# Kernel optimization log

Hardware: AMD Instinct MI355X
Metric: run time of the kernel (lower is better)

Reference implementation:

```python
import jax, jax.numpy as jnp
import numpy as np

# B batch, N seq (n_vec), V vocab, D model dim, H heads, DH head dim,
# L depth, WS window size, R landmark rank, C classes
B, N, V, D, H, DH, L, WS, R, C = 4, 4096, 512, 512, 8, 64, 4, 128, 256, 10
FF = 4 * D
SCALE = DH ** -0.5


def _ln(t, g, b, eps=1e-5):
    mu = jnp.mean(t, axis=-1, keepdims=True)
    var = jnp.var(t, axis=-1, keepdims=True)
    return (t - mu) * jax.lax.rsqrt(var + eps) * g + b


def setup_inputs():
    key = jax.random.key(0)
    ks = iter(jax.random.split(key, 16))

    def w(shape, s=0.02):
        return (jax.random.normal(next(ks), shape) * s).astype(jnp.float32)

    return dict(
        x=jax.random.randint(next(ks), (B, N), 0, V, dtype=jnp.int32),
        tok_emb=w((V, D)), pos_emb=w((N, D)),
        ln1_g=jnp.ones((L, D), jnp.float32), ln1_b=jnp.zeros((L, D), jnp.float32),
        Wq=w((L, D, H * DH)), Wkv=w((L, D, 2 * H * DH)), Wp=w((L, DH, R)),
        lln_g=jnp.ones((L, DH), jnp.float32), lln_b=jnp.zeros((L, DH), jnp.float32),
        gln_g=jnp.ones((L, DH), jnp.float32), gln_b=jnp.zeros((L, DH), jnp.float32),
        Wo=w((L, H * DH, D)), bo=jnp.zeros((L, D), jnp.float32),
        ln2_g=jnp.ones((L, D), jnp.float32), ln2_b=jnp.zeros((L, D), jnp.float32),
        W1=w((L, D, FF)), b1=jnp.zeros((L, FF), jnp.float32),
        W2=w((L, FF, D)), b2=jnp.zeros((L, D), jnp.float32),
        lnf_g=jnp.ones((D,), jnp.float32), lnf_b=jnp.zeros((D,), jnp.float32),
        Wlog=w((D, V)), blog=jnp.zeros((V,), jnp.float32),
        Wfin=w((N * V, C), 0.005), bfin=jnp.zeros((C,), jnp.float32),
    )


def _forward(x, tok_emb, pos_emb, ln1_g, ln1_b, Wq, Wkv, Wp, lln_g, lln_b,
             gln_g, gln_b, Wo, bo, ln2_g, ln2_b, W1, b1, W2, b2,
             lnf_g, lnf_b, Wlog, blog, Wfin, bfin):
    h = tok_emb[x] + pos_emb[None, :, :]  # [B,N,D]
    nw = N // WS
    for l in range(L):
        # ---- PreNorm Long-Short attention ----
        y = _ln(h, ln1_g[l], ln1_b[l])
        q = (y @ Wq[l]).reshape(B, N, H, DH).transpose(0, 2, 1, 3) * SCALE  # [B,H,N,DH]
        kv = (y @ Wkv[l]).reshape(B, N, 2, H, DH).transpose(2, 0, 3, 1, 4)
        k, v = kv[0], kv[1]  # [B,H,N,DH]
        # dynamic low-rank landmark projection: softmax over the sequence dim
        p = jax.nn.softmax(jnp.einsum('bhnd,dr->bhnr', k, Wp[l]), axis=2)
        gk = _ln(jnp.einsum('bhnr,bhnd->bhrd', p, k), gln_g[l], gln_b[l])  # [B,H,R,DH]
        gv = _ln(jnp.einsum('bhnr,bhnd->bhrd', p, v), gln_g[l], gln_b[l])
        # DualLN on the short-range (local window) keys/values
        lk = _ln(k, lln_g[l], lln_b[l]).reshape(B, H, nw, WS, DH)
        lv = _ln(v, lln_g[l], lln_b[l]).reshape(B, H, nw, WS, DH)
        lq = q.reshape(B, H, nw, WS, DH)
        sim_l = jnp.einsum('bhnwd,bhnxd->bhnwx', lq, lk)  # [B,H,nw,WS,WS]
        sim_g = jnp.einsum('bhnwd,bhrd->bhnwr', lq, gk)   # [B,H,nw,WS,R]
        attn = jax.nn.softmax(jnp.concatenate([sim_l, sim_g], axis=-1), axis=-1)
        a_l, a_g = attn[..., :WS], attn[..., WS:]
        o = (jnp.einsum('bhnwx,bhnxd->bhnwd', a_l, lv)
             + jnp.einsum('bhnwr,bhrd->bhnwd', a_g, gv))
        o = o.reshape(B, H, N, DH).transpose(0, 2, 1, 3).reshape(B, N, H * DH)
        h = h + o @ Wo[l] + bo[l]
        # ---- PreNorm FeedForward ----
        y = _ln(h, ln2_g[l], ln2_b[l])
        h = h + jax.nn.gelu(y @ W1[l] + b1[l]) @ W2[l] + b2[l]
    logits = _ln(h, lnf_g, lnf_b) @ Wlog + blog  # [B,N,V]
    # FLATTEN pooling head (dropout is identity in eval mode)
    return logits.reshape(B, N * V) @ Wfin + bfin  # [B,C]


def reference(x, tok_emb, pos_emb, ln1_g, ln1_b, Wq, Wkv, Wp, lln_g, lln_b,
              gln_g, gln_b, Wo, bo, ln2_g, ln2_b, W1, b1, W2, b2,
              lnf_g, lnf_b, Wlog, blog, Wfin, bfin):
    return _forward(x, tok_emb, pos_emb, ln1_g, ln1_b, Wq, Wkv, Wp, lln_g, lln_b,
                    gln_g, gln_b, Wo, bo, ln2_g, ln2_b, W1, b1, W2, b2,
                    lnf_g, lnf_b, Wlog, blog, Wfin, bfin)
```

## Files before the change

### kernel.cpp

```cpp
#include <hip/hip_runtime.h>
#include <hip/hip_bf16.h>

typedef unsigned short u16;
typedef __attribute__((ext_vector_type(8))) short short8;
typedef __attribute__((ext_vector_type(4))) float floatx4;

#define FLAG_GELU   1
#define FLAG_ACC    2
#define FLAG_NN     4
#define FLAG_CF32   8
#define FLAG_ATOMIC 16

__device__ __forceinline__ float bf2f(u16 u){
  union { unsigned u; float f; } c; c.u = ((unsigned)u)<<16; return c.f;
}
__device__ __forceinline__ u16 f2bf(float f){
  union { float f; unsigned u; } c; c.f = f;
  unsigned r = (c.u + 0x7fffu + ((c.u>>16)&1u))>>16;
  return (u16)r;
}
__device__ __forceinline__ float rdin(const void* base, long long idx, int flagv){
  return flagv ? ((const float*)base)[idx] : bf2f(((const u16*)base)[idx]);
}
__device__ __forceinline__ float fast_gelu(float x){
  float u = 0.7978845608028654f*(x + 0.044715f*x*x*x);
  float e = __expf(2.f*u);
  float t = 1.f - 2.f/(e+1.f);
  return 0.5f*x*(1.f+t);
}

__global__ void detect_kernel(const void* tok, int* flag){
  __shared__ int cnt;
  if(threadIdx.x==0) cnt=0;
  __syncthreads();
  float v = fabsf(bf2f(((const u16*)tok)[threadIdx.x]));
  int bad = (v < 1e3f) ? 0 : 1;
  atomicAdd(&cnt, bad);
  __syncthreads();
  if(threadIdx.x==0) *flag = (cnt>0) ? 1 : 0;
}

__global__ void cvtT_kernel(const void* src, long long off0, long long zstride, u16* __restrict__ dst,
    long long dzstride, int K, int N, const int* flag){
  __shared__ float tl[32][33];
  int fl = *flag;
  int k0 = blockIdx.x*32, n0 = blockIdx.y*32;
  long long base = off0 + (long long)blockIdx.z*zstride;
  for(int i=threadIdx.y;i<32;i+=8){
    long long idx = base + (long long)(k0+i)*N + n0 + threadIdx.x;
    tl[i][threadIdx.x] = fl ? ((const float*)src)[idx] : bf2f(((const u16*)src)[idx]);
  }
  __syncthreads();
  u16* dz = dst + (long long)blockIdx.z*dzstride;
  for(int i=threadIdx.y;i<32;i+=8)
    dz[(long long)(n0+i)*K + k0 + threadIdx.x] = f2bf(tl[threadIdx.x][i]);
}

__global__ void transposeB_kernel(const u16* __restrict__ in, u16* __restrict__ out,
    long long izs0, long long izs1, int zd, long long ozstride, int ldin, int ldout){
  __shared__ u16 tl[32][33];
  int z = blockIdx.z; int z0 = z/zd, z1 = z - z0*zd;
  const u16* ip = in + z0*izs0 + z1*izs1;
  u16* op = out + (long long)z*ozstride;
  int r0 = blockIdx.x*32, c0 = blockIdx.y*32;
  for(int i=threadIdx.y;i<32;i+=8)
    tl[i][threadIdx.x] = ip[(long long)(r0+i)*ldin + c0 + threadIdx.x];
  __syncthreads();
  for(int i=threadIdx.y;i<32;i+=8)
    op[(long long)(c0+i)*ldout + r0 + threadIdx.x] = tl[threadIdx.x][i];
}

__global__ __launch_bounds__(256) void zerof_kernel(float* p, int n){
  int i = blockIdx.x*256 + threadIdx.x;
  if(i<n) p[i]=0.f;
}

struct GemmP {
  const u16* A; const u16* B; float* Cf; u16* Ch;
  const void* bias; int biasOff; const int* dflag;
  int K, lda, ldb, ldc;
  long long sA0,sA1,sA2,sB0,sB1,sB2,sC0,sC1,sC2;
  int d0,d1; float alpha; int flags; int ksplit;
};

__global__ __launch_bounds__(256) void gemm_kernel(GemmP p){
  __shared__ __align__(16) u16 As[64][40];
  __shared__ __align__(16) u16 Bs[64][40];
  int z = blockIdx.z;
  int i0 = z / p.d0; int rem = z - i0*p.d0; int i1 = rem / p.d1; int i2 = rem - i1*p.d1;
  const u16* A  = p.A + i0*p.sA0 + i1*p.sA1 + i2*p.sA2;
  const u16* Bp = p.B + i0*p.sB0 + i1*p.sB1 + i2*p.sB2;
  long long cb = i0*p.sC0 + i1*p.sC1 + i2*p.sC2;
  int kbeg = 0, kend = p.K;
  if(p.ksplit){ kbeg = i1*p.ksplit; kend = kbeg + p.ksplit; }
  int m0 = blockIdx.x*64, n0 = blockIdx.y*64;
  int t = threadIdx.x, lane = t&63, wave = t>>6;
  int wm = (wave>>1)*32, wn = (wave&1)*32;
  int quad = lane>>4, l16 = lane&15;
  floatx4 zero4 = {0.f,0.f,0.f,0.f};
  floatx4 acc00=zero4, acc01=zero4, acc10=zero4, acc11=zero4;
  int sr = t>>2, sc = (t&3)*8;
  int bkr = t>>3, bnc = (t&7)*8;
  bool nn = (p.flags & FLAG_NN);
  for(int k0=kbeg;k0<kend;k0+=32){
    uint4 av = *(const uint4*)(A + (long long)(m0+sr)*p.lda + (k0+sc));
    uint4 bv;
    if(nn) bv = *(const uint4*)(Bp + (long long)(k0+bkr)*p.ldb + (n0+bnc));
    else   bv = *(const uint4*)(Bp + (long long)(n0+sr)*p.ldb + (k0+sc));
    *(uint4*)&As[sr][sc] = av;
    if(nn){
      u16 tmp[8]; *(uint4*)tmp = bv;
      #pragma unroll
      for(int j=0;j<8;j++) Bs[bnc+j][bkr] = tmp[j];
    } else {
      *(uint4*)&Bs[sr][sc] = bv;
    }
    __syncthreads();
    short8 a0 = *(const short8*)&As[wm+l16][quad*8];
    short8 a1 = *(const short8*)&As[wm+16+l16][quad*8];
    short8 b0 = *(const short8*)&Bs[wn+l16][quad*8];
    short8 b1 = *(const short8*)&Bs[wn+16+l16][quad*8];
    acc00 = __builtin_amdgcn_mfma_f32_16x16x32_bf16(a0,b0,acc00,0,0,0);
    acc01 = __builtin_amdgcn_mfma_f32_16x16x32_bf16(a0,b1,acc01,0,0,0);
    acc10 = __builtin_amdgcn_mfma_f32_16x16x32_bf16(a1,b0,acc10,0,0,0);
    acc11 = __builtin_amdgcn_mfma_f32_16x16x32_bf16(a1,b1,acc11,0,0,0);
    __syncthreads();
  }
  int flagv = p.bias ? *p.dflag : 0;
  #pragma unroll
  for(int mi=0;mi<2;mi++){
    #pragma unroll
    for(int ni=0;ni<2;ni++){
      floatx4 a = (mi==0)?((ni==0)?acc00:acc01):((ni==0)?acc10:acc11);
      int cg = n0 + wn + ni*16 + l16;
      float bv_ = p.bias ? rdin(p.bias, (long long)p.biasOff + cg, flagv) : 0.f;
      #pragma unroll
      for(int e=0;e<4;e++){
        int rg = m0 + wm + mi*16 + quad*4 + e;
        float v = a[e]*p.alpha + bv_;
        if(p.flags & FLAG_GELU) v = fast_gelu(v);
        long long ci = cb + (long long)rg*p.ldc + cg;
        if(p.flags & FLAG_ATOMIC){
          atomicAdd(&p.Cf[ci], v);
        } else if(p.flags & FLAG_CF32){
          float o2 = v; if(p.flags&FLAG_ACC) o2 += p.Cf[ci];
          p.Cf[ci] = o2;
        } else {
          float o2 = v; if(p.flags&FLAG_ACC) o2 += bf2f(p.Ch[ci]);
          p.Ch[ci] = f2bf(o2);
        }
      }
    }
  }
}

struct Gemm128P {
  const u16* A; const u16* B; float* Cf; u16* Ch;
  const void* bias; int biasOff; const int* dflag;
  int K, lda, ldb, ldc; float alpha; int flags;
};

__global__ __launch_bounds__(256) void gemm128_kernel(Gemm128P p){
  __shared__ __align__(16) u16 lds[17408];
  u16* As = lds;
  u16* Bs = lds + 4096;
  int m0 = blockIdx.x*128, n0 = blockIdx.y*128;
  int t = threadIdx.x, lane = t&63, wave = t>>6;
  int quad = lane>>4, l16 = lane&15;
  int wm = (wave>>1)*64, wn = (wave&1)*64;
  int srow = wave*32 + (lane>>2);
  int skoff = (lane&3)*8;
  const u16* Ag0 = p.A + (long long)(m0+srow)*p.lda + skoff;
  const u16* Ag1 = Ag0 + 16*p.lda;
  const u16* Bg0 = p.B + (long long)(n0+srow)*p.ldb + skoff;
  const u16* Bg1 = Bg0 + 16*p.ldb;
  u16* AsW0 = As + wave*1024;
  u16* AsW1 = AsW0 + 512;
  u16* BsW0 = Bs + wave*1024;
  u16* BsW1 = BsW0 + 512;
  floatx4 acc[4][4] = {};
  for(int k0=0;k0<p.K;k0+=32){
    __builtin_amdgcn_global_load_lds(
      (const __attribute__((address_space(1))) unsigned int*)(Ag0 + k0),
      (__attribute__((address_space(3))) unsigned int*)AsW0, 16, 0, 0);
    __builtin_amdgcn_global_load_lds(
      (const __attribute__((address_space(1))) unsigned int*)(Ag1 + k0),
      (__attribute__((address_space(3))) unsigned int*)AsW1, 16, 0, 0);
    __builtin_amdgcn_global_load_lds(
      (const __attribute__((address_space(1))) unsigned int*)(Bg0 + k0),
      (__attribute__((address_space(3))) unsigned int*)BsW0, 16, 0, 0);
    __builtin_amdgcn_global_load_lds(
      (const __attribute__((address_space(1))) unsigned int*)(Bg1 + k0),
      (__attribute__((address_space(3))) unsigned int*)BsW1, 16, 0, 0);
    __syncthreads();
    short8 af[4], bfr[4];
    #pragma unroll
    for(int i=0;i<4;i++) af[i]  = *(const short8*)&As[(wm+i*16+l16)*32 + quad*8];
    #pragma unroll
    for(int j=0;j<4;j++) bfr[j] = *(const short8*)&Bs[(wn+j*16+l16)*32 + quad*8];
    #pragma unroll
    for(int i=0;i<4;i++)
      #pragma unroll
      for(int j=0;j<4;j++)
        acc[i][j] = __builtin_amdgcn_mfma_f32_16x16x32_bf16(af[i], bfr[j], acc[i][j],0,0,0);
    __syncthreads();
  }
  int flagv = p.bias ? *p.dflag : 0;
  if(!(p.flags & FLAG_CF32)){
    u16* Ct = lds + wave*4352;
    #pragma unroll
    for(int j=0;j<4;j++){
      int cg = n0 + wn + j*16 + l16;
      float bv_ = p.bias ? rdin(p.bias, (long long)p.biasOff + cg, flagv) : 0.f;
      #pragma unroll
      for(int i=0;i<4;i++){
        #pragma unroll
        for(int e=0;e<4;e++){
          float v = acc[i][j][e]*p.alpha + bv_;
          if(p.flags & FLAG_GELU) v = fast_gelu(v);
          Ct[(i*16 + quad*4 + e)*68 + j*16 + l16] = f2bf(v);
        }
      }
    }
    int rsub = lane>>3, csub = (lane&7)*8;
    #pragma unroll
    for(int rr=0; rr<8; rr++){
      int row = rr*8 + rsub;
      uint4 v = *(const uint4*)&Ct[row*68 + csub];
      *(uint4*)(p.Ch + (long long)(m0+wm+row)*p.ldc + (n0+wn+csub)) = v;
    }
  } else {
    #pragma unroll
    for(int j=0;j<4;j++){
      int cg = n0 + wn + j*16 + l16;
      float bv_ = p.bias ? rdin(p.bias, (long long)p.biasOff + cg, flagv) : 0.f;
      #pragma unroll
      for(int i=0;i<4;i++){
        #pragma unroll
        for(int e=0;e<4;e++){
          int rg = m0 + wm + i*16 + quad*4 + e;
          float v = acc[i][j][e]*p.alpha + bv_;
          if(p.flags & FLAG_GELU) v = fast_gelu(v);
          long long ci = (long long)rg*p.ldc + cg;
          float o2 = v; if(p.flags&FLAG_ACC) o2 += p.Cf[ci];
          p.Cf[ci] = o2;
        }
      }
    }
  }
}

struct AttnP {
  const u16* q;
  const u16* k;
  const u16* gk;
  const u16* vT;
  const u16* gvT;
  u16* o;
};

__global__ __launch_bounds__(256) void attn_kernel(AttnP p){
  __shared__ __align__(16) u16 S[4][12544];
  __shared__ float ssum[4][32];
  const int SST = 392;
  int w = blockIdx.x, bh = blockIdx.y;
  int b = bh>>3, hh = bh&7;
  int t = threadIdx.x, lane = t&63, wave = t>>6;
  int quad = lane>>4, l16 = lane&15;
  u16* Sw = &S[wave][0];
  int mbase = w*128 + wave*32;
  short8 aq[2][2];
  #pragma unroll
  for(int mt=0;mt<2;mt++)
    #pragma unroll
    for(int kc=0;kc<2;kc++)
      aq[mt][kc] = *(const short8*)(p.q + ((long long)b*4096 + mbase + mt*16 + l16)*512 + hh*64 + kc*32 + quad*8);
  for(int ct=0; ct<24; ct++){
    short8 bf0, bf1;
    if(ct<8){
      const u16* kr = p.k + ((long long)b*4096 + w*128 + ct*16 + l16)*1024 + hh*64;
      bf0 = *(const short8*)(kr + quad*8);
      bf1 = *(const short8*)(kr + 32 + quad*8);
    } else {
      const u16* gr = p.gk + ((long long)bh*256 + (ct-8)*16 + l16)*64;
      bf0 = *(const short8*)(gr + quad*8);
      bf1 = *(const short8*)(gr + 32 + quad*8);
    }
    #pragma unroll
    for(int mt=0;mt<2;mt++){
      floatx4 acc = {0.f,0.f,0.f,0.f};
      acc = __builtin_amdgcn_mfma_f32_16x16x32_bf16(aq[mt][0], bf0, acc,0,0,0);
      acc = __builtin_amdgcn_mfma_f32_16x16x32_bf16(aq[mt][1], bf1, acc,0,0,0);
      #pragma unroll
      for(int e=0;e<4;e++)
        Sw[(mt*16 + quad*4 + e)*SST + ct*16 + l16] = f2bf(acc[e]);
    }
  }
  __syncthreads();
  {
    int r = lane&31, ph = lane>>5;
    u16* Srow = Sw + r*SST + ph*192;
    float mmax = -3.4e38f;
    u16 buf[8];
    for(int it=0; it<24; it++){
      *(uint4*)buf = *(const uint4*)(Srow + it*8);
      #pragma unroll
      for(int j=0;j<8;j++) mmax = fmaxf(mmax, bf2f(buf[j]));
    }
    mmax = fmaxf(mmax, __shfl_xor(mmax, 32));
    float s = 0.f;
    for(int it=0; it<24; it++){
      *(uint4*)buf = *(const uint4*)(Srow + it*8);
      #pragma unroll
      for(int j=0;j<8;j++){ float e_ = __expf(bf2f(buf[j]) - mmax); s += e_; buf[j] = f2bf(e_); }
      *(uint4*)(Srow + it*8) = *(uint4*)buf;
    }
    s += __shfl_xor(s, 32);
    if(ph==0) ssum[wave][r] = 1.f/s;
  }
  __syncthreads();
  floatx4 oacc[2][4] = {};
  for(int kc=0; kc<12; kc++){
    short8 ap0 = *(const short8*)(Sw + (l16)*SST + kc*32 + quad*8);
    short8 ap1 = *(const short8*)(Sw + (16 + l16)*SST + kc*32 + quad*8);
    #pragma unroll
    for(int dt=0; dt<4; dt++){
      short8 bv;
      if(kc<4)
        bv = *(const short8*)(p.vT + (long long)bh*262144 + (dt*16+l16)*4096 + w*128 + kc*32 + quad*8);
      else
        bv = *(const short8*)(p.gvT + (long long)bh*16384 + (dt*16+l16)*256 + (kc-4)*32 + quad*8);
      oacc[0][dt] = __builtin_amdgcn_mfma_f32_16x16x32_bf16(ap0, bv, oacc[0][dt],0,0,0);
      oacc[1][dt] = __builtin_amdgcn_mfma_f32_16x16x32_bf16(ap1, bv, oacc[1][dt],0,0,0);
    }
  }
  #pragma unroll
  for(int mt=0;mt<2;mt++){
    #pragma unroll
    for(int e=0;e<4;e++){
      int row = mt*16 + quad*4 + e;
      float inv = ssum[wave][row];
      long long obase = ((long long)b*4096 + mbase + row)*512 + hh*64;
      #pragma unroll
      for(int dt=0;dt<4;dt++)
        p.o[obase + dt*16 + l16] = f2bf(oacc[mt][dt][e]*inv);
    }
  }
}

__global__ __launch_bounds__(256) void embed_kernel(const int* __restrict__ x, const void* tok,
    const void* pos, float* __restrict__ h, const int* flag){
  int i = blockIdx.x*256 + threadIdx.x;
  int flagv = *flag;
  int d = i & 511;
  int n = (i>>9) & 4095;
  int bn = i>>9;
  int tid2 = x[bn];
  h[i] = rdin(tok, (long long)tid2*512 + d, flagv) + rdin(pos, (long long)n*512 + d, flagv);
}

__global__ __launch_bounds__(256) void ln512_kernel(const float* __restrict__ h,
    const void* g, const void* b, int goff, u16* __restrict__ y, const int* flag){
  int row = blockIdx.x;
  int flagv = *flag;
  const float* hr = h + (size_t)row*512;
  int t = threadIdx.x;
  float x0 = hr[t], x1 = hr[t+256];
  float s1 = x0+x1, s2 = x0*x0+x1*x1;
  for(int o=32;o>0;o>>=1){ s1 += __shfl_down(s1,o,64); s2 += __shfl_down(s2,o,64); }
  __shared__ float sh1[4], sh2[4];
  int wv=t>>6, ln=t&63;
  if(ln==0){ sh1[wv]=s1; sh2[wv]=s2; }
  __syncthreads();
  float st = sh1[0]+sh1[1]+sh1[2]+sh1[3];
  float qt = sh2[0]+sh2[1]+sh2[2]+sh2[3];
  float mu = st*(1.f/512.f);
  float var = qt*(1.f/512.f) - mu*mu;
  float inv = rsqrtf(var+1e-5f);
  u16* yr = y + (size_t)row*512;
  yr[t]     = f2bf((x0-mu)*inv*rdin(g,goff+t,flagv)     + rdin(b,goff+t,flagv));
  yr[t+256] = f2bf((x1-mu)*inv*rdin(g,goff+t+256,flagv) + rdin(b,goff+t+256,flagv));
}

__global__ __launch_bounds__(256) void ln64_kernel(const u16* __restrict__ in, const float* __restrict__ inF,
    u16* __restrict__ out, const void* g, const void* b, int goff,
    long long s0, long long s1v, long long s2v, int d0, int d1, const int* flag){
  int r = blockIdx.x*4 + (threadIdx.x>>6);
  int ln = threadIdx.x&63;
  int flagv = *flag;
  int i0 = r/d0; int rem = r - i0*d0; int i1 = rem/d1; int i2 = rem - i1*d1;
  long long off = i0*s0 + i1*s1v + i2*s2v;
  float x = inF ? inF[off+ln] : bf2f(in[off + ln]);
  float s = x, sq = x*x;
  for(int o=32;o>0;o>>=1){ s += __shfl_down(s,o,64); sq += __shfl_down(sq,o,64); }
  s = __shfl(s,0,64); sq = __shfl(sq,0,64);
  float mu = s*(1.f/64.f), var = sq*(1.f/64.f)-mu*mu;
  float inv = rsqrtf(var+1e-5f);
  out[off + ln] = f2bf((x-mu)*inv*rdin(g,goff+ln,flagv) + rdin(b,goff+ln,flagv));
}

__global__ __launch_bounds__(256) void softmax4096_kernel(u16* __restrict__ p){
  u16* pr = p + (size_t)blockIdx.x*4096;
  int t = threadIdx.x;
  u16 tmp[16];
  *(uint4*)tmp     = *(const uint4*)(pr + t*16);
  *(uint4*)(tmp+8) = *(const uint4*)(pr + t*16 + 8);
  float xs[16]; float m=-3.4e38f;
  #pragma unroll
  for(int i=0;i<16;i++){ xs[i]=bf2f(tmp[i]); m=fmaxf(m,xs[i]); }
  for(int o=32;o>0;o>>=1) m = fmaxf(m, __shfl_down(m,o,64));
  __shared__ float sm[4]; __shared__ float sv[4];
  int wv=t>>6, ln=t&63;
  if(ln==0) sm[wv]=m;
  __syncthreads();
  m = fmaxf(fmaxf(sm[0],sm[1]),fmaxf(sm[2],sm[3]));
  float s=0;
  #pragma unroll
  for(int i=0;i<16;i++){ xs[i]=__expf(xs[i]-m); s+=xs[i]; }
  for(int o=32;o>0;o>>=1) s += __shfl_down(s,o,64);
  if(ln==0) sv[wv]=s;
  __syncthreads();
  s = sv[0]+sv[1]+sv[2]+sv[3];
  float inv = 1.f/s;
  #pragma unroll
  for(int i=0;i<16;i++) tmp[i]=f2bf(xs[i]*inv);
  *(uint4*)(pr + t*16)     = *(uint4*)tmp;
  *(uint4*)(pr + t*16 + 8) = *(uint4*)(tmp+8);
}

__global__ void zero40_kernel(float* p){ if(threadIdx.x<40) p[threadIdx.x]=0.f; }

__global__ __launch_bounds__(256) void head_kernel(const float* __restrict__ logits,
    const void* wfin, float* __restrict__ part, const int* flag){
  int b = blockIdx.x>>7, chunk = blockIdx.x&127;
  int flagv = *flag;
  const float* lr = logits + (size_t)b*2097152 + (size_t)chunk*16384;
  float acc[10];
  #pragma unroll
  for(int c=0;c<10;c++) acc[c]=0.f;
  for(int j=threadIdx.x;j<16384;j+=256){
    float lv_ = lr[j];
    long long wb = (long long)(chunk*16384 + j)*10;
    if(flagv){
      const float* w = (const float*)wfin + wb;
      #pragma unroll
      for(int c=0;c<10;c++) acc[c] += lv_*w[c];
    } else {
      const u16* w = (const u16*)wfin + wb;
      #pragma unroll
      for(int c=0;c<10;c++) acc[c] += lv_*bf2f(w[c]);
    }
  }
  __shared__ float red[4];
  int wv=threadIdx.x>>6, ln=threadIdx.x&63;
  for(int c=0;c<10;c++){
    float v=acc[c];
    for(int o=32;o>0;o>>=1) v+=__shfl_down(v,o,64);
    __syncthreads();
    if(ln==0) red[wv]=v;
    __syncthreads();
    if(threadIdx.x==0) atomicAdd(&part[b*10+c], red[0]+red[1]+red[2]+red[3]);
  }
}

__global__ void fin_kernel(const float* __restrict__ part, const void* bfin, void* out, const int* flag){
  int i=threadIdx.x;
  int flagv = *flag;
  if(i<40){
    float r = part[i] + rdin(bfin, i%10, flagv);
    if(flagv) ((float*)out)[i] = r;
    else      ((u16*)out)[i]   = f2bf(r);
  }
}

static const size_t OFF_H    = 0;
static const size_t OFF_Y    = 33554432;
static const size_t OFF_GKF  = 33554432;
static const size_t OFF_GVF  = 35651584;
static const size_t OFF_Q    = 50331648;
static const size_t OFF_KV   = 67108864;
static const size_t OFF_GK   = 100663296;
static const size_t OFF_GV   = 101711872;
static const size_t OFF_BIG  = 102760448;
static const size_t OFF_KT   = 169869312;
static const size_t OFF_VT   = 186646528;
static const size_t OFF_WTP  = 203423744;
static const size_t OFF_WQT  = 203554816;
static const size_t OFF_WKVT = 204079104;
static const size_t OFF_WOT  = 205127680;
static const size_t OFF_W1T  = 205651968;
static const size_t OFF_W2T  = 207749120;
static const size_t OFF_PART = 209846272;
static const size_t OFF_FLAG = 209846528;
static const size_t WS_NEED  = 209846784;

static inline GemmP mkg(const void*A,const void*B,void*C,const void*bias,int biasOff,const int* dflag,
  int K,int lda,int ldb,int ldc,
  long long a0,long long a1,long long a2,long long b0,long long b1,long long b2,
  long long c0,long long c1,long long c2,int d0,int d1,float alpha,int flags,int ksplit){
  GemmP p; p.A=(const u16*)A; p.B=(const u16*)B;
  p.Cf=(float*)C; p.Ch=(u16*)C; p.bias=bias; p.biasOff=biasOff; p.dflag=dflag;
  p.K=K;p.lda=lda;p.ldb=ldb;p.ldc=ldc;
  p.sA0=a0;p.sA1=a1;p.sA2=a2;p.sB0=b0;p.sB1=b1;p.sB2=b2;p.sC0=c0;p.sC1=c1;p.sC2=c2;
  p.d0=d0;p.d1=d1;p.alpha=alpha;p.flags=flags;p.ksplit=ksplit; return p;
}
static inline Gemm128P mk128(const void*A,const void*B,void*C,const void*bias,int biasOff,const int* dflag,
  int K,int lda,int ldb,int ldc,float alpha,int flags){
  Gemm128P p; p.A=(const u16*)A; p.B=(const u16*)B;
  p.Cf=(float*)C; p.Ch=(u16*)C; p.bias=bias; p.biasOff=biasOff; p.dflag=dflag;
  p.K=K;p.lda=lda;p.ldb=ldb;p.ldc=ldc;p.alpha=alpha;p.flags=flags; return p;
}

extern "C" void kernel_launch(void* const* d_in, const int* in_sizes, int n_in,
                              void* d_out, int out_size, void* d_ws, size_t ws_size,
                              hipStream_t stream){
  (void)in_sizes;(void)n_in;(void)out_size;
  if(ws_size < WS_NEED) return;
  const int*  x    = (const int*)d_in[0];
  const void* tok  = d_in[1];
  const void* pos  = d_in[2];
  const void* ln1g = d_in[3];
  const void* ln1b = d_in[4];
  const void* Wq   = d_in[5];
  const void* Wkv  = d_in[6];
  const void* Wp   = d_in[7];
  const void* llng = d_in[8];
  const void* llnb = d_in[9];
  const void* glng = d_in[10];
  const void* glnb = d_in[11];
  const void* Wo   = d_in[12];
  const void* bo   = d_in[13];
  const void* ln2g = d_in[14];
  const void* ln2b = d_in[15];
  const void* W1   = d_in[16];
  const void* b1   = d_in[17];
  const void* W2   = d_in[18];
  const void* b2   = d_in[19];
  const void* lnfg = d_in[20];
  const void* lnfb = d_in[21];
  const void* Wlog = d_in[22];
  const void* blog = d_in[23];
  const void* Wfin = d_in[24];
  const void* bfin = d_in[25];

  char* ws = (char*)d_ws;
  float* h    = (float*)(ws + OFF_H);
  u16* y      = (u16*)(ws + OFF_Y);
  u16* ob     = (u16*)(ws + OFF_Y);
  float* gkF  = (float*)(ws + OFF_GKF);
  float* gvF  = (float*)(ws + OFF_GVF);
  u16* qb     = (u16*)(ws + OFF_Q);
  u16* kv     = (u16*)(ws + OFF_KV);
  u16* gk     = (u16*)(ws + OFF_GK);
  u16* gv     = (u16*)(ws + OFF_GV);
  u16* big    = (u16*)(ws + OFF_BIG);
  float* bigf = (float*)(ws + OFF_BIG);
  u16* kT     = (u16*)(ws + OFF_KT);
  u16* gvT    = (u16*)(ws + OFF_KT);
  u16* vT     = (u16*)(ws + OFF_VT);
  u16* wTp    = (u16*)(ws + OFF_WTP);
  u16* sWqT   = (u16*)(ws + OFF_WQT);
  u16* sWkvT  = (u16*)(ws + OFF_WKVT);
  u16* sWoT   = (u16*)(ws + OFF_WOT);
  u16* sW1T   = (u16*)(ws + OFF_W1T);
  u16* sW2T   = (u16*)(ws + OFF_W2T);
  float* part = (float*)(ws + OFF_PART);
  int* flag   = (int*)(ws + OFF_FLAG);

  dim3 tb(32,8);
  detect_kernel<<<dim3(1),dim3(256),0,stream>>>(tok, flag);
  cvtT_kernel<<<dim3(2,8,4),tb,0,stream>>>(Wp, 0, 16384, wTp, 16384, 64, 256, flag);
  embed_kernel<<<dim3(32768),dim3(256),0,stream>>>(x, tok, pos, h, flag);

  for(int l=0;l<4;l++){
    cvtT_kernel<<<dim3(16,16,1),tb,0,stream>>>(Wq,  (long long)l*262144,  0, sWqT,  0, 512, 512,  flag);
    cvtT_kernel<<<dim3(16,32,1),tb,0,stream>>>(Wkv, (long long)l*524288,  0, sWkvT, 0, 512, 1024, flag);
    cvtT_kernel<<<dim3(16,16,1),tb,0,stream>>>(Wo,  (long long)l*262144,  0, sWoT,  0, 512, 512,  flag);
    cvtT_kernel<<<dim3(16,64,1),tb,0,stream>>>(W1,  (long long)l*1048576, 0, sW1T,  0, 512, 2048, flag);
    cvtT_kernel<<<dim3(64,16,1),tb,0,stream>>>(W2,  (long long)l*1048576, 0, sW2T,  0, 2048, 512, flag);

    ln512_kernel<<<dim3(16384),dim3(256),0,stream>>>(h, ln1g, ln1b, l*512, y, flag);
    { Gemm128P p = mk128(y, sWqT, qb, nullptr,0,flag, 512,512,512,512, 0.125f, 0);
      gemm128_kernel<<<dim3(128,4),256,0,stream>>>(p); }
    { Gemm128P p = mk128(y, sWkvT, kv, nullptr,0,flag, 512,512,512,1024, 1.f, 0);
      gemm128_kernel<<<dim3(128,8),256,0,stream>>>(p); }
    zerof_kernel<<<dim3(4096),dim3(256),0,stream>>>(gkF, 1048576);
    { GemmP p = mkg(wTp + (size_t)l*16384, kv, big, nullptr,0,flag, 64,64,1024,4096,
        0,0,0, 4194304LL,64,0, 8388608LL,1048576LL,0, 8,1, 1.f, 0, 0);
      gemm_kernel<<<dim3(4,64,32),256,0,stream>>>(p); }
    softmax4096_kernel<<<dim3(8192),dim3(256),0,stream>>>(big);
    transposeB_kernel<<<dim3(128,2,32),tb,0,stream>>>(kv,     kT, 4194304LL,64,8, 262144LL, 1024, 4096);
    transposeB_kernel<<<dim3(128,2,32),tb,0,stream>>>(kv+512, vT, 4194304LL,64,8, 262144LL, 1024, 4096);
    { GemmP p = mkg(big, kT, gkF, nullptr,0,flag, 4096,4096,4096,64,
        1048576LL,0,0, 262144LL,0,0, 16384LL,0,0, 8,1, 1.f, FLAG_CF32|FLAG_ATOMIC, 512);
      gemm_kernel<<<dim3(4,1,256),256,0,stream>>>(p); }
    { GemmP p = mkg(big, vT, gvF, nullptr,0,flag, 4096,4096,4096,64,
        1048576LL,0,0, 262144LL,0,0, 16384LL,0,0, 8,1, 1.f, FLAG_CF32|FLAG_ATOMIC, 512);
      gemm_kernel<<<dim3(4,1,256),256,0,stream>>>(p); }
    ln64_kernel<<<dim3(2048),dim3(256),0,stream>>>(gk, gkF, gk, glng, glnb, l*64, 64,1,1, 1,1, flag);
    ln64_kernel<<<dim3(2048),dim3(256),0,stream>>>(gv, gvF, gv, glng, glnb, l*64, 64,1,1, 1,1, flag);
    ln64_kernel<<<dim3(32768),dim3(256),0,stream>>>(kv,     nullptr, kv,     llng, llnb, l*64, 4194304LL,64,1024, 32768,4096, flag);
    ln64_kernel<<<dim3(32768),dim3(256),0,stream>>>(kv+512, nullptr, kv+512, llng, llnb, l*64, 4194304LL,64,1024, 32768,4096, flag);
    transposeB_kernel<<<dim3(128,2,32),tb,0,stream>>>(kv+512, vT, 4194304LL,64,8, 262144LL, 1024, 4096);
    transposeB_kernel<<<dim3(8,2,32),tb,0,stream>>>(gv, gvT, 16384LL,0,1, 16384LL, 64, 256);
    { AttnP ap; ap.q=qb; ap.k=kv; ap.gk=gk; ap.vT=vT; ap.gvT=gvT; ap.o=ob;
      attn_kernel<<<dim3(32,32),256,0,stream>>>(ap); }
    { Gemm128P p = mk128(ob, sWoT, h, bo,l*512,flag, 512,512,512,512, 1.f, FLAG_ACC|FLAG_CF32);
      gemm128_kernel<<<dim3(128,4),256,0,stream>>>(p); }
    ln512_kernel<<<dim3(16384),dim3(256),0,stream>>>(h, ln2g, ln2b, l*512, y, flag);
    { Gemm128P p = mk128(y, sW1T, big, b1,l*2048,flag, 512,512,512,2048, 1.f, FLAG_GELU);
      gemm128_kernel<<<dim3(128,16),256,0,stream>>>(p); }
    { Gemm128P p = mk128(big, sW2T, h, b2,l*512,flag, 2048,2048,2048,512, 1.f, FLAG_ACC|FLAG_CF32);
      gemm128_kernel<<<dim3(128,4),256,0,stream>>>(p); }
  }
  ln512_kernel<<<dim3(16384),dim3(256),0,stream>>>(h, lnfg, lnfb, 0, y, flag);
  cvtT_kernel<<<dim3(16,16,1),tb,0,stream>>>(Wlog, 0, 0, sWqT, 0, 512, 512, flag);
  { Gemm128P p = mk128(y, sWqT, bigf, blog,0,flag, 512,512,512,512, 1.f, FLAG_CF32);
    gemm128_kernel<<<dim3(128,4),256,0,stream>>>(p); }
  zero40_kernel<<<dim3(1),dim3(64),0,stream>>>(part);
  head_kernel<<<dim3(512),dim3(256),0,stream>>>(bigf, Wfin, part, flag);
  fin_kernel<<<dim3(1),dim3(64),0,stream>>>(part, bfin, d_out, flag);
}
```

Measured before the change: 2.644 ms.

## Replace dense GEMMs with double-buffered 512-thread kernel using larger tiles

Replaces the single-buffered 128x128 GEMM with a templated kernel that uses 8 waves, a 256-wide N tile and BM of 128 or 256, plus a K step of 64. It double-buffers the LDS tiles, so the next K slice loads asynchronously while MFMAs run on the current one, and it needs one barrier per iteration instead of two. Larger tiles improve operand reuse and cut global traffic per FLOP. In exchange, the grids are smaller, leaving fewer blocks to fill the CUs, and LDS use is higher (up to about 136KB for BM=256), which limits occupancy.

```diff
diff --git a/kernel.cpp b/kernel.cpp
--- a/kernel.cpp
+++ b/kernel.cpp
@@ -160,60 +160,79 @@
   int K, lda, ldb, ldc; float alpha; int flags;
 };
 
-__global__ __launch_bounds__(256) void gemm128_kernel(Gemm128P p){
-  __shared__ __align__(16) u16 lds[17408];
+template<int BM>
+__global__ __launch_bounds__(512) void gemm2ph_kernel(Gemm128P p){
+  constexpr int NA   = BM/64;
+  constexpr int HH   = BM/2;
+  constexpr int MI   = HH/16;
+  constexpr int ABUF = BM*64;
+  constexpr int LDSZ = (BM==256) ? 69632 : 49152;
+  __shared__ __align__(16) u16 lds[LDSZ];
   u16* As = lds;
-  u16* Bs = lds + 4096;
-  int m0 = blockIdx.x*128, n0 = blockIdx.y*128;
+  u16* Bs = lds + 2*ABUF;
+  int m0 = blockIdx.x*BM, n0 = blockIdx.y*256;
   int t = threadIdx.x, lane = t&63, wave = t>>6;
   int quad = lane>>4, l16 = lane&15;
-  int wm = (wave>>1)*64, wn = (wave&1)*64;
-  int srow = wave*32 + (lane>>2);
-  int skoff = (lane&3)*8;
-  const u16* Ag0 = p.A + (long long)(m0+srow)*p.lda + skoff;
-  const u16* Ag1 = Ag0 + 16*p.lda;
-  const u16* Bg0 = p.B + (long long)(n0+srow)*p.ldb + skoff;
-  const u16* Bg1 = Bg0 + 16*p.ldb;
-  u16* AsW0 = As + wave*1024;
-  u16* AsW1 = AsW0 + 512;
-  u16* BsW0 = Bs + wave*1024;
-  u16* BsW1 = BsW0 + 512;
-  floatx4 acc[4][4] = {};
-  for(int k0=0;k0<p.K;k0+=32){
-    __builtin_amdgcn_global_load_lds(
-      (const __attribute__((address_space(1))) unsigned int*)(Ag0 + k0),
-      (__attribute__((address_space(3))) unsigned int*)AsW0, 16, 0, 0);
-    __builtin_amdgcn_global_load_lds(
-      (const __attribute__((address_space(1))) unsigned int*)(Ag1 + k0),
-      (__attribute__((address_space(3))) unsigned int*)AsW1, 16, 0, 0);
-    __builtin_amdgcn_global_load_lds(
-      (const __attribute__((address_space(1))) unsigned int*)(Bg0 + k0),
-      (__attribute__((address_space(3))) unsigned int*)BsW0, 16, 0, 0);
-    __builtin_amdgcn_global_load_lds(
-      (const __attribute__((address_space(1))) unsigned int*)(Bg1 + k0),
-      (__attribute__((address_space(3))) unsigned int*)BsW1, 16, 0, 0);
+  int wr = wave>>2, wc = wave&3;
+  int rowA = t>>3, colk = (t&7)*8;
+  const u16* Asrc[NA];
+  const u16* Bsrc[4];
+  #pragma unroll
+  for(int q=0;q<NA;q++) Asrc[q] = p.A + (long long)(m0 + q*64 + rowA)*p.lda + colk;
+  #pragma unroll
+  for(int q=0;q<4;q++)  Bsrc[q] = p.B + (long long)(n0 + q*64 + rowA)*p.ldb + colk;
+  int nk = p.K >> 6;
+  floatx4 acc[MI][4] = {};
+
+  auto stage = [&](int buf, int k0){
+    #pragma unroll
+    for(int q=0;q<NA;q++)
+      __builtin_amdgcn_global_load_lds(
+        (const __attribute__((address_space(1))) unsigned int*)(Asrc[q] + k0),
+        (__attribute__((address_space(3))) unsigned int*)(As + buf*ABUF + q*4096 + wave*512),
+        16, 0, 0);
+    #pragma unroll
+    for(int q=0;q<4;q++)
+      __builtin_amdgcn_global_load_lds(
+        (const __attribute__((address_space(1))) unsigned int*)(Bsrc[q] + k0),
+        (__attribute__((address_space(3))) unsigned int*)(Bs + buf*16384 + q*4096 + wave*512),
+        16, 0, 0);
+  };
+
+  stage(0, 0);
+  __syncthreads();
+  for(int kt=0; kt<nk; ++kt){
+    int cur = kt&1;
+    if(kt+1 < nk) stage(cur^1, (kt+1)*64);
+    const u16* Ab = As + cur*ABUF;
+    const u16* Bb = Bs + cur*16384;
+    #pragma unroll
+    for(int ks=0; ks<2; ks++){
+      short8 a[MI], b[4];
+      #pragma unroll
+      for(int i=0;i<MI;i++)
+        a[i] = *(const short8*)&Ab[(wr*HH + i*16 + l16)*64 + ks*32 + quad*8];
+      #pragma unroll
+      for(int j=0;j<4;j++)
+        b[j] = *(const short8*)&Bb[(wc*64 + j*16 + l16)*64 + ks*32 + quad*8];
+      #pragma unroll
+      for(int i=0;i<MI;i++)
+        #pragma unroll
+        for(int j=0;j<4;j++)
+          acc[i][j] = __builtin_amdgcn_mfma_f32_16x16x32_bf16(a[i], b[j], acc[i][j],0,0,0);
+    }
     __syncthreads();
-    short8 af[4], bfr[4];
-    #pragma unroll
-    for(int i=0;i<4;i++) af[i]  = *(const short8*)&As[(wm+i*16+l16)*32 + quad*8];
-    #pragma unroll
-    for(int j=0;j<4;j++) bfr[j] = *(const short8*)&Bs[(wn+j*16+l16)*32 + quad*8];
-    #pragma unroll
-    for(int i=0;i<4;i++)
-      #pragma unroll
-      for(int j=0;j<4;j++)
-        acc[i][j] = __builtin_amdgcn_mfma_f32_16x16x32_bf16(af[i], bfr[j], acc[i][j],0,0,0);
-    __syncthreads();
-  }
+  }
+
   int flagv = p.bias ? *p.dflag : 0;
   if(!(p.flags & FLAG_CF32)){
-    u16* Ct = lds + wave*4352;
+    u16* Ct = lds + wave*(HH*68);
     #pragma unroll
     for(int j=0;j<4;j++){
-      int cg = n0 + wn + j*16 + l16;
+      int cg = n0 + wc*64 + j*16 + l16;
       float bv_ = p.bias ? rdin(p.bias, (long long)p.biasOff + cg, flagv) : 0.f;
       #pragma unroll
-      for(int i=0;i<4;i++){
+      for(int i=0;i<MI;i++){
         #pragma unroll
         for(int e=0;e<4;e++){
           float v = acc[i][j][e]*p.alpha + bv_;
@@ -224,21 +243,21 @@
     }
     int rsub = lane>>3, csub = (lane&7)*8;
     #pragma unroll
-    for(int rr=0; rr<8; rr++){
+    for(int rr=0; rr<HH/8; rr++){
       int row = rr*8 + rsub;
       uint4 v = *(const uint4*)&Ct[row*68 + csub];
-      *(uint4*)(p.Ch + (long long)(m0+wm+row)*p.ldc + (n0+wn+csub)) = v;
+      *(uint4*)(p.Ch + (long long)(m0 + wr*HH + row)*p.ldc + (n0 + wc*64 + csub)) = v;
     }
   } else {
     #pragma unroll
     for(int j=0;j<4;j++){
-      int cg = n0 + wn + j*16 + l16;
+      int cg = n0 + wc*64 + j*16 + l16;
       float bv_ = p.bias ? rdin(p.bias, (long long)p.biasOff + cg, flagv) : 0.f;
       #pragma unroll
-      for(int i=0;i<4;i++){
+      for(int i=0;i<MI;i++){
         #pragma unroll
         for(int e=0;e<4;e++){
-          int rg = m0 + wm + i*16 + quad*4 + e;
+          int rg = m0 + wr*HH + i*16 + quad*4 + e;
           float v = acc[i][j][e]*p.alpha + bv_;
           if(p.flags & FLAG_GELU) v = fast_gelu(v);
           long long ci = (long long)rg*p.ldc + cg;
@@ -581,9 +600,9 @@
 
     ln512_kernel<<<dim3(16384),dim3(256),0,stream>>>(h, ln1g, ln1b, l*512, y, flag);
     { Gemm128P p = mk128(y, sWqT, qb, nullptr,0,flag, 512,512,512,512, 0.125f, 0);
-      gemm128_kernel<<<dim3(128,4),256,0,stream>>>(p); }
+      gemm2ph_kernel<128><<<dim3(128,2),512,0,stream>>>(p); }
     { Gemm128P p = mk128(y, sWkvT, kv, nullptr,0,flag, 512,512,512,1024, 1.f, 0);
-      gemm128_kernel<<<dim3(128,8),256,0,stream>>>(p); }
+      gemm2ph_kernel<256><<<dim3(64,4),512,0,stream>>>(p); }
     zerof_kernel<<<dim3(4096),dim3(256),0,stream>>>(gkF, 1048576);
     { GemmP p = mkg(wTp + (size_t)l*16384, kv, big, nullptr,0,flag, 64,64,1024,4096,
         0,0,0, 4194304LL,64,0, 8388608LL,1048576LL,0, 8,1, 1.f, 0, 0);
@@ -606,17 +625,17 @@
     { AttnP ap; ap.q=qb; ap.k=kv; ap.gk=gk; ap.vT=vT; ap.gvT=gvT; ap.o=ob;
       attn_kernel<<<dim3(32,32),256,0,stream>>>(ap); }
     { Gemm128P p = mk128(ob, sWoT, h, bo,l*512,flag, 512,512,512,512, 1.f, FLAG_ACC|FLAG_CF32);
-      gemm128_kernel<<<dim3(128,4),256,0,stream>>>(p); }
+      gemm2ph_kernel<128><<<dim3(128,2),512,0,stream>>>(p); }
     ln512_kernel<<<dim3(16384),dim3(256),0,stream>>>(h, ln2g, ln2b, l*512, y, flag);
     { Gemm128P p = mk128(y, sW1T, big, b1,l*2048,flag, 512,512,512,2048, 1.f, FLAG_GELU);
-      gemm128_kernel<<<dim3(128,16),256,0,stream>>>(p); }
+      gemm2ph_kernel<256><<<dim3(64,8),512,0,stream>>>(p); }
     { Gemm128P p = mk128(big, sW2T, h, b2,l*512,flag, 2048,2048,2048,512, 1.f, FLAG_ACC|FLAG_CF32);
-      gemm128_kernel<<<dim3(128,4),256,0,stream>>>(p); }
+      gemm2ph_kernel<128><<<dim3(128,2),512,0,stream>>>(p); }
   }
   ln512_kernel<<<dim3(16384),dim3(256),0,stream>>>(h, lnfg, lnfb, 0, y, flag);
   cvtT_kernel<<<dim3(16,16,1),tb,0,stream>>>(Wlog, 0, 0, sWqT, 0, 512, 512, flag);
   { Gemm128P p = mk128(y, sWqT, bigf, blog,0,flag, 512,512,512,512, 1.f, FLAG_CF32);
-    gemm128_kernel<<<dim3(128,4),256,0,stream>>>(p); }
+    gemm2ph_kernel<128><<<dim3(128,2),512,0,stream>>>(p); }
   zero40_kernel<<<dim3(1),dim3(64),0,stream>>>(part);
   head_kernel<<<dim3(512),dim3(256),0,stream>>>(bigf, Wfin, part, flag);
   fin_kernel<<<dim3(1),dim3(64),0,stream>>>(part, bfin, d_out, flag);
```

Result: faster. 2.559 ms (-3.2%).
